# Optimization experiments

Measured on AMD Instinct MI355X. Metric: run time of the kernel, lower is better.

Reference implementation:

```python
import jax, jax.numpy as jnp
import numpy as np

STATE_BITS = 10          # L: bits of trellis state
SHIFT_BITS = 2           # K: bits shifted in per step -> 2^K predecessors
CHUNK = 4                # chunk_size: values emitted per trellis step
S = 1 << STATE_BITS      # number of states (codebook rows)
NPRED = 1 << SHIFT_BITS  # predecessors per state
HI = 1 << (STATE_BITS - SHIFT_BITS)


def setup_inputs() -> dict:
    key = jax.random.key(0)
    k1, k2 = jax.random.split(key)
    array = jax.random.normal(k1, (1024, 1024), dtype=jnp.float32)
    codebook = jax.random.normal(k2, (S, CHUNK), dtype=jnp.float32)
    return {"array": array, "codebook": codebook, "block_size": 16}


def _viterbi(x, codebook):
    # x: [T, CHUNK, B] target chunks; codebook: [S, CHUNK]
    # Exact min-squared-error Viterbi over the bit-shift trellis:
    #   next_state = ((prev << K) | new_bits) mod 2^L
    # Predecessors of state s: (s >> K) + j * 2^(L-K), j in [0, 2^K)
    s = jnp.arange(S)
    prev_idx = (s[:, None] >> SHIFT_BITS) + jnp.arange(NPRED)[None, :] * HI  # [S, NPRED]
    cnorm = jnp.sum(codebook * codebook, axis=1)  # [S]

    def cost(xt):  # xt: [CHUNK, B] -> [S, B] squared distances
        return cnorm[:, None] - 2.0 * (codebook @ xt) + jnp.sum(xt * xt, axis=0)[None, :]

    alpha0 = cost(x[0])  # free initial state: cost of emitting first chunk

    def step(alpha, xt):
        cand = alpha[prev_idx]                        # [S, NPRED, B]
        j = jnp.argmin(cand, axis=1)                  # [S, B]
        alpha_new = jnp.min(cand, axis=1) + cost(xt)  # [S, B]
        return alpha_new, j.astype(jnp.int8)

    alpha_T, bps = jax.lax.scan(step, alpha0, x[1:])  # bps: [T-1, S, B] int8
    last = jnp.argmin(alpha_T, axis=0).astype(jnp.int32)  # [B] state at step T-1

    def back(state, bp):
        # state: [B] state at step t; bp: [S, B] backpointers into step t
        j = jnp.take_along_axis(bp, state[None, :], axis=0)[0].astype(jnp.int32)
        prev = (state >> SHIFT_BITS) + j * HI
        return prev, state

    first, rest = jax.lax.scan(back, last, bps, reverse=True)
    return jnp.concatenate([first[None], rest], axis=0)  # [T, B] int32


def reference(array, codebook, block_size):
    rows, columns = array.shape
    br, bc = rows // block_size, columns // block_size
    epb = block_size * block_size          # elements_per_block
    T = epb // CHUNK                       # number_of_steps
    B = br * bc                            # number_of_blocks
    # block reshape: [rows, cols] -> [elements_per_block, number_of_blocks]
    blocks = (array.reshape(br, block_size, bc, block_size)
                   .transpose(0, 2, 1, 3)
                   .reshape(B, epb).T)
    x = blocks.reshape(T, CHUNK, B)
    states = _viterbi(x, codebook)         # [T, B]
    vals = codebook[states]                # [T, B, CHUNK] gather reconstruct
    rec = vals.transpose(0, 2, 1).reshape(epb, B)
    rec = (rec.T.reshape(br, bc, block_size, block_size)
              .transpose(0, 2, 1, 3)
              .reshape(rows, columns))
    states_out = states.T.reshape(br, bc, T)
    return rec, states_out
```

## Files before the change

### kernel.cpp

```cpp
#include <hip/hip_runtime.h>


#define COLS      1024
#define T_STEPS   64
#define REC_SIZE  (1024 * 1024)

__global__ __launch_bounds__(128)
__attribute__((amdgpu_waves_per_eu(4, 4)))
void viterbi_q(
    const float* __restrict__ arr,
    const float* __restrict__ cbook,
    float* __restrict__ out)
{
    const int tid   = threadIdx.x;
    const int wid   = tid >> 6;
    const int lane  = tid & 63;
    const int chain = (blockIdx.x << 1) | wid;
    const int rb    = chain >> 6;
    const int cb    = chain & 63;

    __shared__ __align__(16) float tile[2][256];
    __shared__ __align__(16) float Mst[2][256];
    __shared__ unsigned char Jb[2][63 * 64];
    __shared__ int st_lds[2][64];

    {
        const int r  = lane >> 2;
        const int c4 = (lane & 3) << 2;
        float4 v = *(const float4*)(arr + (rb * 16 + r) * COLS + cb * 16 + c4);
        *(float4*)&tile[wid][lane << 2] = v;
    }
    *(float4*)&Mst[wid][lane << 2] = make_float4(0.f, 0.f, 0.f, 0.f);

    float4 a[16];
    float  h[16];
    #pragma unroll
    for (int j = 0; j < 4; ++j) {
        #pragma unroll
        for (int c = 0; c < 4; ++c) {
            const int row = (lane << 2) + c + (j << 8);
            float4 v = *(const float4*)(cbook + row * 4);
            a[j * 4 + c] = v;
            h[j * 4 + c] = -0.5f * (v.x * v.x + v.y * v.y +
                                    v.z * v.z + v.w * v.w);
        }
    }

    const float* __restrict__ tilep = &tile[wid][0];
    float* __restrict__ Mp          = &Mst[wid][0];
    unsigned char* __restrict__ Jp  = &Jb[wid][0];

    #pragma unroll 1
    for (int t = 0; t < T_STEPS - 1; ++t) {
        const float4 xt = *(const float4*)&tilep[t << 2];
        float mj[4];
        #pragma unroll
        for (int j = 0; j < 4; ++j)
            mj[j] = Mp[lane + 64 * j];

        float nm[4];
        unsigned bp = 0;
        #pragma unroll
        for (int c = 0; c < 4; ++c) {
            float cand[4];
            #pragma unroll
            for (int j = 0; j < 4; ++j) {
                const float4 av = a[j * 4 + c];
                float acc = fmaf(av.x, xt.x, h[j * 4 + c]);
                acc = fmaf(av.y, xt.y, acc);
                acc = fmaf(av.z, xt.z, acc);
                acc = fmaf(av.w, xt.w, acc);
                cand[j] = acc + mj[j];
            }
            const float v = fmaxf(fmaxf(fmaxf(cand[0], cand[1]), cand[2]),
                                  cand[3]);
            const int j = (cand[0] == v) ? 0
                        : (cand[1] == v) ? 1
                        : (cand[2] == v) ? 2 : 3;
            nm[c] = v;
            bp |= (unsigned)j << (2 * c);
        }
        *(float4*)&Mp[lane << 2] = make_float4(nm[0], nm[1], nm[2], nm[3]);
        Jp[t * 64 + lane] = (unsigned char)bp;
    }

    int bests;
    {
        const int t = T_STEPS - 1;
        const float4 xt = *(const float4*)&tilep[t << 2];
        float mj[4];
        #pragma unroll
        for (int j = 0; j < 4; ++j)
            mj[j] = Mp[lane + 64 * j];

        float bv = -3.4e38f;
        int   bs = 0;
        #pragma unroll
        for (int j = 0; j < 4; ++j) {
            #pragma unroll
            for (int c = 0; c < 4; ++c) {
                const float4 av = a[j * 4 + c];
                float acc = fmaf(av.x, xt.x, h[j * 4 + c]);
                acc = fmaf(av.y, xt.y, acc);
                acc = fmaf(av.z, xt.z, acc);
                acc = fmaf(av.w, xt.w, acc);
                acc += mj[j];
                if (acc > bv) { bv = acc; bs = (lane << 2) + c + (j << 8); }
            }
        }
        #pragma unroll
        for (int off = 32; off > 0; off >>= 1) {
            const float ov = __shfl_xor(bv, off, 64);
            const int   os = __shfl_xor(bs, off, 64);
            if (ov > bv || (ov == bv && os < bs)) { bv = ov; bs = os; }
        }
        bests = bs;
    }

    if (lane == 0) {
        int s = bests;
        st_lds[wid][T_STEPS - 1] = s;
        for (int i = T_STEPS - 2; i >= 0; --i) {
            const int p = s >> 2;
            const unsigned byte = Jp[i * 64 + (p >> 2)];
            const int j = (byte >> (2 * (p & 3))) & 3;
            s = p + (j << 8);
            st_lds[wid][i] = s;
        }
    }

    const int st = st_lds[wid][lane];
    out[REC_SIZE + chain * 64 + lane] = (float)st;
    const float4 v = *(const float4*)(cbook + st * 4);
    const int r  = lane >> 2;
    const int c4 = (lane & 3) << 2;
    *(float4*)(out + (rb * 16 + r) * COLS + cb * 16 + c4) = v;
}

extern "C" void kernel_launch(void* const* d_in, const int* in_sizes, int n_in,
                              void* d_out, int out_size, void* d_ws, size_t ws_size,
                              hipStream_t stream)
{
    const float* arr   = (const float*)d_in[0];
    const float* cbook = (const float*)d_in[1];
    float* out = (float*)d_out;
    viterbi_q<<<dim3(2048), dim3(128), 0, stream>>>(arr, cbook, out);
}
```

Measured before the change: 104.8 us.

## Process two Viterbi chains per wavefront to share codebook registers

Each 64-lane wavefront now runs two independent block chains interleaved, instead of one chain per wave in a 128-thread block. The codebook registers (a, h) are loaded once and reused for both chains, and the two independent dependency chains give more instruction-level parallelism within the serial time loop. The cost is half the number of waves (2048 single-wave blocks), more registers per wave, and occupancy limited to two waves per EU, which may reduce latency hiding.

```diff
diff --git a/kernel.cpp b/kernel.cpp
--- a/kernel.cpp
+++ b/kernel.cpp
@@ -5,19 +5,18 @@
 #define T_STEPS   64
 #define REC_SIZE  (1024 * 1024)
 
-__global__ __launch_bounds__(128)
-__attribute__((amdgpu_waves_per_eu(4, 4)))
+__global__ __launch_bounds__(64)
+__attribute__((amdgpu_waves_per_eu(2, 2)))
 void viterbi_q(
     const float* __restrict__ arr,
     const float* __restrict__ cbook,
     float* __restrict__ out)
 {
-    const int tid   = threadIdx.x;
-    const int wid   = tid >> 6;
-    const int lane  = tid & 63;
-    const int chain = (blockIdx.x << 1) | wid;
-    const int rb    = chain >> 6;
-    const int cb    = chain & 63;
+    const int lane = threadIdx.x & 63;
+    const int cA   = blockIdx.x << 1;
+    const int cB   = cA | 1;
+    const int rbA  = cA >> 6, cbA = cA & 63;
+    const int rbB  = cB >> 6, cbB = cB & 63;
 
     __shared__ __align__(16) float tile[2][256];
     __shared__ __align__(16) float Mst[2][256];
@@ -27,10 +26,13 @@
     {
         const int r  = lane >> 2;
         const int c4 = (lane & 3) << 2;
-        float4 v = *(const float4*)(arr + (rb * 16 + r) * COLS + cb * 16 + c4);
-        *(float4*)&tile[wid][lane << 2] = v;
+        float4 vA = *(const float4*)(arr + (rbA * 16 + r) * COLS + cbA * 16 + c4);
+        float4 vB = *(const float4*)(arr + (rbB * 16 + r) * COLS + cbB * 16 + c4);
+        *(float4*)&tile[0][lane << 2] = vA;
+        *(float4*)&tile[1][lane << 2] = vB;
     }
-    *(float4*)&Mst[wid][lane << 2] = make_float4(0.f, 0.f, 0.f, 0.f);
+    *(float4*)&Mst[0][lane << 2] = make_float4(0.f, 0.f, 0.f, 0.f);
+    *(float4*)&Mst[1][lane << 2] = make_float4(0.f, 0.f, 0.f, 0.f);
 
     float4 a[16];
     float  h[16];
@@ -46,95 +48,144 @@
         }
     }
 
-    const float* __restrict__ tilep = &tile[wid][0];
-    float* __restrict__ Mp          = &Mst[wid][0];
-    unsigned char* __restrict__ Jp  = &Jb[wid][0];
+    const float* __restrict__ tA = &tile[0][0];
+    const float* __restrict__ tB = &tile[1][0];
+    float* __restrict__ MA       = &Mst[0][0];
+    float* __restrict__ MB       = &Mst[1][0];
+    unsigned char* __restrict__ JA = &Jb[0][0];
+    unsigned char* __restrict__ JB = &Jb[1][0];
 
     #pragma unroll 1
     for (int t = 0; t < T_STEPS - 1; ++t) {
-        const float4 xt = *(const float4*)&tilep[t << 2];
-        float mj[4];
+        const float4 xtA = *(const float4*)&tA[t << 2];
+        const float4 xtB = *(const float4*)&tB[t << 2];
+        float mjA[4], mjB[4];
         #pragma unroll
-        for (int j = 0; j < 4; ++j)
-            mj[j] = Mp[lane + 64 * j];
+        for (int j = 0; j < 4; ++j) mjA[j] = MA[lane + 64 * j];
+        #pragma unroll
+        for (int j = 0; j < 4; ++j) mjB[j] = MB[lane + 64 * j];
 
-        float nm[4];
-        unsigned bp = 0;
+        float nmA[4];
+        unsigned bpA = 0;
         #pragma unroll
         for (int c = 0; c < 4; ++c) {
             float cand[4];
             #pragma unroll
             for (int j = 0; j < 4; ++j) {
                 const float4 av = a[j * 4 + c];
-                float acc = fmaf(av.x, xt.x, h[j * 4 + c]);
-                acc = fmaf(av.y, xt.y, acc);
-                acc = fmaf(av.z, xt.z, acc);
-                acc = fmaf(av.w, xt.w, acc);
-                cand[j] = acc + mj[j];
+                float acc = fmaf(av.x, xtA.x, h[j * 4 + c]);
+                acc = fmaf(av.y, xtA.y, acc);
+                acc = fmaf(av.z, xtA.z, acc);
+                acc = fmaf(av.w, xtA.w, acc);
+                cand[j] = acc + mjA[j];
             }
             const float v = fmaxf(fmaxf(fmaxf(cand[0], cand[1]), cand[2]),
                                   cand[3]);
             const int j = (cand[0] == v) ? 0
                         : (cand[1] == v) ? 1
                         : (cand[2] == v) ? 2 : 3;
-            nm[c] = v;
-            bp |= (unsigned)j << (2 * c);
+            nmA[c] = v;
+            bpA |= (unsigned)j << (2 * c);
         }
-        *(float4*)&Mp[lane << 2] = make_float4(nm[0], nm[1], nm[2], nm[3]);
-        Jp[t * 64 + lane] = (unsigned char)bp;
+
+        float nmB[4];
+        unsigned bpB = 0;
+        #pragma unroll
+        for (int c = 0; c < 4; ++c) {
+            float cand[4];
+            #pragma unroll
+            for (int j = 0; j < 4; ++j) {
+                const float4 av = a[j * 4 + c];
+                float acc = fmaf(av.x, xtB.x, h[j * 4 + c]);
+                acc = fmaf(av.y, xtB.y, acc);
+                acc = fmaf(av.z, xtB.z, acc);
+                acc = fmaf(av.w, xtB.w, acc);
+                cand[j] = acc + mjB[j];
+            }
+            const float v = fmaxf(fmaxf(fmaxf(cand[0], cand[1]), cand[2]),
+                                  cand[3]);
+            const int j = (cand[0] == v) ? 0
+                        : (cand[1] == v) ? 1
+                        : (cand[2] == v) ? 2 : 3;
+            nmB[c] = v;
+            bpB |= (unsigned)j << (2 * c);
+        }
+
+        *(float4*)&MA[lane << 2] = make_float4(nmA[0], nmA[1], nmA[2], nmA[3]);
+        *(float4*)&MB[lane << 2] = make_float4(nmB[0], nmB[1], nmB[2], nmB[3]);
+        JA[t * 64 + lane] = (unsigned char)bpA;
+        JB[t * 64 + lane] = (unsigned char)bpB;
     }
 
-    int bests;
+    int bestsA, bestsB;
     {
         const int t = T_STEPS - 1;
-        const float4 xt = *(const float4*)&tilep[t << 2];
-        float mj[4];
+        const float4 xtA = *(const float4*)&tA[t << 2];
+        const float4 xtB = *(const float4*)&tB[t << 2];
+        float mjA[4], mjB[4];
         #pragma unroll
-        for (int j = 0; j < 4; ++j)
-            mj[j] = Mp[lane + 64 * j];
+        for (int j = 0; j < 4; ++j) mjA[j] = MA[lane + 64 * j];
+        #pragma unroll
+        for (int j = 0; j < 4; ++j) mjB[j] = MB[lane + 64 * j];
 
-        float bv = -3.4e38f;
-        int   bs = 0;
+        float bvA = -3.4e38f, bvB = -3.4e38f;
+        int   bsA = 0,        bsB = 0;
         #pragma unroll
         for (int j = 0; j < 4; ++j) {
             #pragma unroll
             for (int c = 0; c < 4; ++c) {
                 const float4 av = a[j * 4 + c];
-                float acc = fmaf(av.x, xt.x, h[j * 4 + c]);
-                acc = fmaf(av.y, xt.y, acc);
-                acc = fmaf(av.z, xt.z, acc);
-                acc = fmaf(av.w, xt.w, acc);
-                acc += mj[j];
-                if (acc > bv) { bv = acc; bs = (lane << 2) + c + (j << 8); }
+                float accA = fmaf(av.x, xtA.x, h[j * 4 + c]);
+                accA = fmaf(av.y, xtA.y, accA);
+                accA = fmaf(av.z, xtA.z, accA);
+                accA = fmaf(av.w, xtA.w, accA);
+                accA += mjA[j];
+                if (accA > bvA) { bvA = accA; bsA = (lane << 2) + c + (j << 8); }
+
+                float accB = fmaf(av.x, xtB.x, h[j * 4 + c]);
+                accB = fmaf(av.y, xtB.y, accB);
+                accB = fmaf(av.z, xtB.z, accB);
+                accB = fmaf(av.w, xtB.w, accB);
+                accB += mjB[j];
+                if (accB > bvB) { bvB = accB; bsB = (lane << 2) + c + (j << 8); }
             }
         }
         #pragma unroll
         for (int off = 32; off > 0; off >>= 1) {
-            const float ov = __shfl_xor(bv, off, 64);
-            const int   os = __shfl_xor(bs, off, 64);
-            if (ov > bv || (ov == bv && os < bs)) { bv = ov; bs = os; }
+            const float ovA = __shfl_xor(bvA, off, 64);
+            const int   osA = __shfl_xor(bsA, off, 64);
+            const float ovB = __shfl_xor(bvB, off, 64);
+            const int   osB = __shfl_xor(bsB, off, 64);
+            if (ovA > bvA || (ovA == bvA && osA < bsA)) { bvA = ovA; bsA = osA; }
+            if (ovB > bvB || (ovB == bvB && osB < bsB)) { bvB = ovB; bsB = osB; }
         }
-        bests = bs;
+        bestsA = bsA;
+        bestsB = bsB;
     }
 
-    if (lane == 0) {
-        int s = bests;
-        st_lds[wid][T_STEPS - 1] = s;
+    if (lane < 2) {
+        const unsigned char* __restrict__ Jp = (lane == 0) ? JA : JB;
+        int s = (lane == 0) ? bestsA : bestsB;
+        st_lds[lane][T_STEPS - 1] = s;
         for (int i = T_STEPS - 2; i >= 0; --i) {
             const int p = s >> 2;
             const unsigned byte = Jp[i * 64 + (p >> 2)];
             const int j = (byte >> (2 * (p & 3))) & 3;
             s = p + (j << 8);
-            st_lds[wid][i] = s;
+            st_lds[lane][i] = s;
         }
     }
 
-    const int st = st_lds[wid][lane];
-    out[REC_SIZE + chain * 64 + lane] = (float)st;
-    const float4 v = *(const float4*)(cbook + st * 4);
+    const int stA = st_lds[0][lane];
+    const int stB = st_lds[1][lane];
+    out[REC_SIZE + cA * 64 + lane] = (float)stA;
+    out[REC_SIZE + cB * 64 + lane] = (float)stB;
+    const float4 vA = *(const float4*)(cbook + stA * 4);
+    const float4 vB = *(const float4*)(cbook + stB * 4);
     const int r  = lane >> 2;
     const int c4 = (lane & 3) << 2;
-    *(float4*)(out + (rb * 16 + r) * COLS + cb * 16 + c4) = v;
+    *(float4*)(out + (rbA * 16 + r) * COLS + cbA * 16 + c4) = vA;
+    *(float4*)(out + (rbB * 16 + r) * COLS + cbB * 16 + c4) = vB;
 }
 
 extern "C" void kernel_launch(void* const* d_in, const int* in_sizes, int n_in,
@@ -144,5 +195,5 @@
     const float* arr   = (const float*)d_in[0];
     const float* cbook = (const float*)d_in[1];
     float* out = (float*)d_out;
-    viterbi_q<<<dim3(2048), dim3(128), 0, stream>>>(arr, cbook, out);
+    viterbi_q<<<dim3(2048), dim3(64), 0, stream>>>(arr, cbook, out);
 }
```

Result: slower. 115.0 us (+9.7%).

## Spread each Viterbi chain across a 256-thread block, one state per thread

Applied to the files above, without the earlier changes.

Each block of 256 threads now handles a single block chain, with each thread owning one trellis state instead of one wave handling 1024 states at 16 per lane. The path metrics are double-buffered in LDS with a block barrier per step, backpointers are stored as one byte per state, and the final argmax is reduced across waves through shared memory. This cuts per-thread register use and serial work per step, raising parallelism and occupancy. The cost is 63 block-wide barriers per chain, more LDS traffic for metrics and backpointers, and idle threads during load, traceback and store.

```diff
diff --git a/kernel.cpp b/kernel.cpp
--- a/kernel.cpp
+++ b/kernel.cpp
@@ -5,108 +5,92 @@
 #define T_STEPS   64
 #define REC_SIZE  (1024 * 1024)
 
-__global__ __launch_bounds__(128)
-__attribute__((amdgpu_waves_per_eu(4, 4)))
+__global__ __launch_bounds__(256)
+__attribute__((amdgpu_waves_per_eu(4, 8)))
 void viterbi_q(
     const float* __restrict__ arr,
     const float* __restrict__ cbook,
     float* __restrict__ out)
 {
     const int tid   = threadIdx.x;
+    const int lane  = tid & 63;
     const int wid   = tid >> 6;
-    const int lane  = tid & 63;
-    const int chain = (blockIdx.x << 1) | wid;
+    const int chain = blockIdx.x;
     const int rb    = chain >> 6;
     const int cb    = chain & 63;
 
-    __shared__ __align__(16) float tile[2][256];
-    __shared__ __align__(16) float Mst[2][256];
-    __shared__ unsigned char Jb[2][63 * 64];
-    __shared__ int st_lds[2][64];
+    __shared__ __align__(16) float tile[256];
+    __shared__ __align__(16) float Mbuf[2][256];
+    __shared__ unsigned char J[63 * 256];
+    __shared__ int   st_lds[64];
+    __shared__ float redv[4];
+    __shared__ int   reds[4];
+
+    if (tid < 64) {
+        const int r  = tid >> 2;
+        const int c4 = (tid & 3) << 2;
+        float4 v = *(const float4*)(arr + (rb * 16 + r) * COLS + cb * 16 + c4);
+        *(float4*)&tile[tid << 2] = v;
+    }
+    Mbuf[0][tid] = 0.f;
+
+    float4 a[4];
+    float  h[4];
+    #pragma unroll
+    for (int j = 0; j < 4; ++j) {
+        float4 v = *(const float4*)(cbook + (tid + (j << 8)) * 4);
+        a[j] = v;
+        h[j] = -0.5f * (v.x * v.x + v.y * v.y + v.z * v.z + v.w * v.w);
+    }
+
+    __syncthreads();
+
+#define STEP(T, RB, WB)                                                       \
+    {                                                                         \
+        const float4 xt = *(const float4*)&tile[(T) << 2];                    \
+        float cand[4];                                                        \
+        _Pragma("unroll")                                                     \
+        for (int j = 0; j < 4; ++j) {                                         \
+            const float m = Mbuf[RB][(tid >> 2) + (j << 6)];                  \
+            float acc = fmaf(a[j].x, xt.x, h[j]);                             \
+            acc = fmaf(a[j].y, xt.y, acc);                                    \
+            acc = fmaf(a[j].z, xt.z, acc);                                    \
+            acc = fmaf(a[j].w, xt.w, acc);                                    \
+            cand[j] = acc + m;                                                \
+        }                                                                     \
+        const float v = fmaxf(fmaxf(fmaxf(cand[0], cand[1]), cand[2]),        \
+                              cand[3]);                                       \
+        const int jidx = (cand[0] == v) ? 0                                   \
+                       : (cand[1] == v) ? 1                                   \
+                       : (cand[2] == v) ? 2 : 3;                              \
+        Mbuf[WB][tid] = v;                                                    \
+        J[(T) * 256 + tid] = (unsigned char)jidx;                             \
+    }
+
+    #pragma unroll 1
+    for (int t = 0; t < 62; t += 2) {
+        STEP(t, 0, 1);
+        __syncthreads();
+        STEP(t + 1, 1, 0);
+        __syncthreads();
+    }
+    STEP(62, 0, 1);
+    __syncthreads();
+#undef STEP
 
     {
-        const int r  = lane >> 2;
-        const int c4 = (lane & 3) << 2;
-        float4 v = *(const float4*)(arr + (rb * 16 + r) * COLS + cb * 16 + c4);
-        *(float4*)&tile[wid][lane << 2] = v;
-    }
-    *(float4*)&Mst[wid][lane << 2] = make_float4(0.f, 0.f, 0.f, 0.f);
-
-    float4 a[16];
-    float  h[16];
-    #pragma unroll
-    for (int j = 0; j < 4; ++j) {
-        #pragma unroll
-        for (int c = 0; c < 4; ++c) {
-            const int row = (lane << 2) + c + (j << 8);
-            float4 v = *(const float4*)(cbook + row * 4);
-            a[j * 4 + c] = v;
-            h[j * 4 + c] = -0.5f * (v.x * v.x + v.y * v.y +
-                                    v.z * v.z + v.w * v.w);
-        }
-    }
-
-    const float* __restrict__ tilep = &tile[wid][0];
-    float* __restrict__ Mp          = &Mst[wid][0];
-    unsigned char* __restrict__ Jp  = &Jb[wid][0];
-
-    #pragma unroll 1
-    for (int t = 0; t < T_STEPS - 1; ++t) {
-        const float4 xt = *(const float4*)&tilep[t << 2];
-        float mj[4];
-        #pragma unroll
-        for (int j = 0; j < 4; ++j)
-            mj[j] = Mp[lane + 64 * j];
-
-        float nm[4];
-        unsigned bp = 0;
-        #pragma unroll
-        for (int c = 0; c < 4; ++c) {
-            float cand[4];
-            #pragma unroll
-            for (int j = 0; j < 4; ++j) {
-                const float4 av = a[j * 4 + c];
-                float acc = fmaf(av.x, xt.x, h[j * 4 + c]);
-                acc = fmaf(av.y, xt.y, acc);
-                acc = fmaf(av.z, xt.z, acc);
-                acc = fmaf(av.w, xt.w, acc);
-                cand[j] = acc + mj[j];
-            }
-            const float v = fmaxf(fmaxf(fmaxf(cand[0], cand[1]), cand[2]),
-                                  cand[3]);
-            const int j = (cand[0] == v) ? 0
-                        : (cand[1] == v) ? 1
-                        : (cand[2] == v) ? 2 : 3;
-            nm[c] = v;
-            bp |= (unsigned)j << (2 * c);
-        }
-        *(float4*)&Mp[lane << 2] = make_float4(nm[0], nm[1], nm[2], nm[3]);
-        Jp[t * 64 + lane] = (unsigned char)bp;
-    }
-
-    int bests;
-    {
-        const int t = T_STEPS - 1;
-        const float4 xt = *(const float4*)&tilep[t << 2];
-        float mj[4];
-        #pragma unroll
-        for (int j = 0; j < 4; ++j)
-            mj[j] = Mp[lane + 64 * j];
-
+        const float4 xt = *(const float4*)&tile[63 << 2];
         float bv = -3.4e38f;
         int   bs = 0;
         #pragma unroll
         for (int j = 0; j < 4; ++j) {
-            #pragma unroll
-            for (int c = 0; c < 4; ++c) {
-                const float4 av = a[j * 4 + c];
-                float acc = fmaf(av.x, xt.x, h[j * 4 + c]);
-                acc = fmaf(av.y, xt.y, acc);
-                acc = fmaf(av.z, xt.z, acc);
-                acc = fmaf(av.w, xt.w, acc);
-                acc += mj[j];
-                if (acc > bv) { bv = acc; bs = (lane << 2) + c + (j << 8); }
-            }
+            const float m = Mbuf[1][(tid >> 2) + (j << 6)];
+            float acc = fmaf(a[j].x, xt.x, h[j]);
+            acc = fmaf(a[j].y, xt.y, acc);
+            acc = fmaf(a[j].z, xt.z, acc);
+            acc = fmaf(a[j].w, xt.w, acc);
+            acc += m;
+            if (acc > bv) { bv = acc; bs = tid + (j << 8); }
         }
         #pragma unroll
         for (int off = 32; off > 0; off >>= 1) {
@@ -114,27 +98,39 @@
             const int   os = __shfl_xor(bs, off, 64);
             if (ov > bv || (ov == bv && os < bs)) { bv = ov; bs = os; }
         }
-        bests = bs;
+        if (lane == 0) { redv[wid] = bv; reds[wid] = bs; }
     }
+    __syncthreads();
 
-    if (lane == 0) {
-        int s = bests;
-        st_lds[wid][T_STEPS - 1] = s;
+    if (tid == 0) {
+        float gv = redv[0];
+        int   gs = reds[0];
+        #pragma unroll
+        for (int w = 1; w < 4; ++w) {
+            if (redv[w] > gv || (redv[w] == gv && reds[w] < gs)) {
+                gv = redv[w];
+                gs = reds[w];
+            }
+        }
+        int s = gs;
+        st_lds[T_STEPS - 1] = s;
         for (int i = T_STEPS - 2; i >= 0; --i) {
             const int p = s >> 2;
-            const unsigned byte = Jp[i * 64 + (p >> 2)];
-            const int j = (byte >> (2 * (p & 3))) & 3;
+            const int j = J[i * 256 + p];
             s = p + (j << 8);
-            st_lds[wid][i] = s;
+            st_lds[i] = s;
         }
     }
+    __syncthreads();
 
-    const int st = st_lds[wid][lane];
-    out[REC_SIZE + chain * 64 + lane] = (float)st;
-    const float4 v = *(const float4*)(cbook + st * 4);
-    const int r  = lane >> 2;
-    const int c4 = (lane & 3) << 2;
-    *(float4*)(out + (rb * 16 + r) * COLS + cb * 16 + c4) = v;
+    if (tid < 64) {
+        const int st = st_lds[tid];
+        out[REC_SIZE + chain * 64 + tid] = (float)st;
+        const float4 v = *(const float4*)(cbook + st * 4);
+        const int r  = tid >> 2;
+        const int c4 = (tid & 3) << 2;
+        *(float4*)(out + (rb * 16 + r) * COLS + cb * 16 + c4) = v;
+    }
 }
 
 extern "C" void kernel_launch(void* const* d_in, const int* in_sizes, int n_in,
@@ -144,5 +140,5 @@
     const float* arr   = (const float*)d_in[0];
     const float* cbook = (const float*)d_in[1];
     float* out = (float*)d_out;
-    viterbi_q<<<dim3(2048), dim3(128), 0, stream>>>(arr, cbook, out);
+    viterbi_q<<<dim3(4096), dim3(256), 0, stream>>>(arr, cbook, out);
 }
```

New measurement: 110.1 us. 1.05x slower.

## Keep Viterbi path metrics in registers and gather predecessors via ds_bpermute

Applied to the files above, without the earlier changes.

Remaps trellis states to lanes so each lane's predecessors sit in a single lane per slot, then fetches predecessor metrics with ds_bpermute instead of writing and re-reading an LDS metric array each step. This removes the per-step LDS store/load round trip on the recurrence's critical path. In exchange it issues 16 cross-lane permutes per step, and the backtrack indexing is adjusted to the new byte layout.

```diff
diff --git a/kernel.cpp b/kernel.cpp
--- a/kernel.cpp
+++ b/kernel.cpp
@@ -20,7 +20,6 @@
     const int cb    = chain & 63;
 
     __shared__ __align__(16) float tile[2][256];
-    __shared__ __align__(16) float Mst[2][256];
     __shared__ unsigned char Jb[2][63 * 64];
     __shared__ int st_lds[2][64];
 
@@ -30,82 +29,90 @@
         float4 v = *(const float4*)(arr + (rb * 16 + r) * COLS + cb * 16 + c4);
         *(float4*)&tile[wid][lane << 2] = v;
     }
-    *(float4*)&Mst[wid][lane << 2] = make_float4(0.f, 0.f, 0.f, 0.f);
 
     float4 a[16];
     float  h[16];
     #pragma unroll
-    for (int j = 0; j < 4; ++j) {
+    for (int i = 0; i < 4; ++i) {
         #pragma unroll
-        for (int c = 0; c < 4; ++c) {
-            const int row = (lane << 2) + c + (j << 8);
+        for (int j = 0; j < 4; ++j) {
+            const int row = lane + (i << 6) + (j << 8);
             float4 v = *(const float4*)(cbook + row * 4);
-            a[j * 4 + c] = v;
-            h[j * 4 + c] = -0.5f * (v.x * v.x + v.y * v.y +
-                                    v.z * v.z + v.w * v.w);
+            a[(i << 2) | j] = v;
+            h[(i << 2) | j] = -0.5f * (v.x * v.x + v.y * v.y +
+                                       v.z * v.z + v.w * v.w);
         }
     }
 
+    int ba[4];
+    #pragma unroll
+    for (int i = 0; i < 4; ++i)
+        ba[i] = ((lane >> 2) + (i << 4)) << 2;
+
     const float* __restrict__ tilep = &tile[wid][0];
-    float* __restrict__ Mp          = &Mst[wid][0];
     unsigned char* __restrict__ Jp  = &Jb[wid][0];
+
+    float mprev[4] = {0.f, 0.f, 0.f, 0.f};
+
+#define FETCH_MM(MM)                                                          \
+    _Pragma("unroll")                                                         \
+    for (int i = 0; i < 4; ++i) {                                             \
+        _Pragma("unroll")                                                     \
+        for (int j = 0; j < 4; ++j)                                           \
+            (MM)[(i << 2) | j] = __int_as_float(                              \
+                __builtin_amdgcn_ds_bpermute(ba[i],                           \
+                                             __float_as_int(mprev[j])));      \
+    }
 
     #pragma unroll 1
     for (int t = 0; t < T_STEPS - 1; ++t) {
+        float mm[16];
+        FETCH_MM(mm)
         const float4 xt = *(const float4*)&tilep[t << 2];
-        float mj[4];
-        #pragma unroll
-        for (int j = 0; j < 4; ++j)
-            mj[j] = Mp[lane + 64 * j];
 
-        float nm[4];
         unsigned bp = 0;
         #pragma unroll
-        for (int c = 0; c < 4; ++c) {
+        for (int i = 0; i < 4; ++i) {
             float cand[4];
             #pragma unroll
             for (int j = 0; j < 4; ++j) {
-                const float4 av = a[j * 4 + c];
-                float acc = fmaf(av.x, xt.x, h[j * 4 + c]);
+                const float4 av = a[(i << 2) | j];
+                float acc = fmaf(av.x, xt.x, h[(i << 2) | j]);
                 acc = fmaf(av.y, xt.y, acc);
                 acc = fmaf(av.z, xt.z, acc);
                 acc = fmaf(av.w, xt.w, acc);
-                cand[j] = acc + mj[j];
+                cand[j] = acc + mm[(i << 2) | j];
             }
             const float v = fmaxf(fmaxf(fmaxf(cand[0], cand[1]), cand[2]),
                                   cand[3]);
             const int j = (cand[0] == v) ? 0
                         : (cand[1] == v) ? 1
                         : (cand[2] == v) ? 2 : 3;
-            nm[c] = v;
-            bp |= (unsigned)j << (2 * c);
+            mprev[i] = v;
+            bp |= (unsigned)j << (2 * i);
         }
-        *(float4*)&Mp[lane << 2] = make_float4(nm[0], nm[1], nm[2], nm[3]);
         Jp[t * 64 + lane] = (unsigned char)bp;
     }
 
     int bests;
     {
-        const int t = T_STEPS - 1;
-        const float4 xt = *(const float4*)&tilep[t << 2];
-        float mj[4];
-        #pragma unroll
-        for (int j = 0; j < 4; ++j)
-            mj[j] = Mp[lane + 64 * j];
+        float mm[16];
+        FETCH_MM(mm)
+        const float4 xt = *(const float4*)&tilep[63 << 2];
 
         float bv = -3.4e38f;
         int   bs = 0;
         #pragma unroll
         for (int j = 0; j < 4; ++j) {
             #pragma unroll
-            for (int c = 0; c < 4; ++c) {
-                const float4 av = a[j * 4 + c];
-                float acc = fmaf(av.x, xt.x, h[j * 4 + c]);
+            for (int i = 0; i < 4; ++i) {
+                const float4 av = a[(i << 2) | j];
+                float acc = fmaf(av.x, xt.x, h[(i << 2) | j]);
                 acc = fmaf(av.y, xt.y, acc);
                 acc = fmaf(av.z, xt.z, acc);
                 acc = fmaf(av.w, xt.w, acc);
-                acc += mj[j];
-                if (acc > bv) { bv = acc; bs = (lane << 2) + c + (j << 8); }
+                acc += mm[(i << 2) | j];
+                if (acc > bv) { bv = acc; bs = lane + (i << 6) + (j << 8); }
             }
         }
         #pragma unroll
@@ -116,14 +123,15 @@
         }
         bests = bs;
     }
+#undef FETCH_MM
 
     if (lane == 0) {
         int s = bests;
         st_lds[wid][T_STEPS - 1] = s;
         for (int i = T_STEPS - 2; i >= 0; --i) {
             const int p = s >> 2;
-            const unsigned byte = Jp[i * 64 + (p >> 2)];
-            const int j = (byte >> (2 * (p & 3))) & 3;
+            const unsigned byte = Jp[i * 64 + (p & 63)];
+            const int j = (byte >> (2 * (p >> 6))) & 3;
             s = p + (j << 8);
             st_lds[wid][i] = s;
         }
```

Result: slower. 119.3 us (+13.8%).
